# Performance work log

Measured on AMD Instinct MI355X. Metric: run time of the kernel, lower is better.

## Reference

```python
import jax, jax.numpy as jnp
import numpy as np

K = 5  # Chebyshev order


def laplacian(w):
    # normalized Laplacian: I - D^{-1/2} W D^{-1/2}
    d = jnp.sum(w, axis=1)
    d_re = 1.0 / jnp.sqrt(d + 1e-5)
    return jnp.eye(w.shape[0], dtype=w.dtype) - d_re[:, None] * w * d_re[None, :]


def cheb_terms(x, lap, k):
    # x: [B,N,C], lap: [N,N] -> [B,k,N,C]
    # Faithful to torch code: T0 = ones, then (x, lap@x) recurrence for k>2.
    t0 = jnp.ones_like(x)
    if k == 1:
        return t0[:, None]
    t1 = jnp.matmul(lap, x)
    if k == 2:
        return jnp.stack([t0, t1], axis=1)
    terms = [t0, x, t1]
    tkm1, tk = x, t1
    for _ in range(3, k):
        tkm1, tk = tk, 2.0 * jnp.matmul(lap, tk) - tkm1
        terms.append(tk)
    return jnp.stack(terms, axis=1)


def graph_conv(x, lap, w, k):
    # torch: cp.permute(0,2,3,1).flatten(2) @ w, i.e. flat index = c*k + t
    t = cheb_terms(x, lap, k)                       # [B,k,N,C]
    C = x.shape[-1]
    O = w.shape[-1]
    return jnp.einsum('bknc,cko->bno', t, w.reshape(C, k, O))


def setup_inputs() -> dict:
    key = jax.random.key(0)
    ks = jax.random.split(key, 9)
    B, N, Cin, H = 8192, 32, 60, 128
    return {
        'x': jax.random.normal(ks[0], (B, N, Cin), dtype=jnp.float32),
        'adj': jax.random.normal(ks[1], (N, N), dtype=jnp.float32) * 0.1,
        'adj_bias': jax.random.normal(ks[2], (1,), dtype=jnp.float32) * 0.1 + 0.2,
        'w1': jax.random.normal(ks[3], (K * Cin, H), dtype=jnp.float32) * 0.05,
        'b1': jax.random.normal(ks[4], (1, 1, H), dtype=jnp.float32) * 0.05,
        'w2': jax.random.normal(ks[5], (K * H, H), dtype=jnp.float32) * 0.05,
        'b2': jax.random.normal(ks[6], (1, 1, H), dtype=jnp.float32) * 0.05,
        'fc_w': jax.random.normal(ks[7], (2, N * H), dtype=jnp.float32) * 0.02,
        'fc_b': jax.random.normal(ks[8], (2,), dtype=jnp.float32) * 0.02,
    }


def reference(x, adj, adj_bias, w1, b1, w2, b2, fc_w, fc_b):
    # DGCNN.forward (eval mode: dropout = identity)
    a = jax.nn.relu(adj + adj_bias)
    lap = laplacian(a)
    h = graph_conv(x, lap, w1, K)
    h = jax.nn.relu(h + b1)      # B1ReLU
    h = graph_conv(h, lap, w2, K)
    h = jax.nn.relu(h + b2)
    h = h.reshape(h.shape[0], -1)  # [B, N*H]
    return h @ fc_w.T + fc_b
```

## Files before the change

### kernel.cpp

```cpp
#include <hip/hip_runtime.h>

typedef unsigned short u16;
typedef short bf16x8 __attribute__((ext_vector_type(8)));
typedef short short4v __attribute__((ext_vector_type(4)));
typedef float f32x4 __attribute__((ext_vector_type(4)));

#define MFMA16(a, b, c) __builtin_amdgcn_mfma_f32_16x16x32_bf16((a), (b), (c), 0, 0, 0)

__device__ __forceinline__ u16 f2bf(float f) {
  unsigned u = __builtin_bit_cast(unsigned, f);
  u += 0x7FFFu + ((u >> 16) & 1u);
  return (u16)(u >> 16);
}

#define WS_MGF   0
#define WS_WT1F  8192
#define WS_WT2F  73728
#define WS_B1    204800
#define WS_B2    205312

__global__ void prep_kernel(const float* __restrict__ adj,
                            const float* __restrict__ adj_bias,
                            const float* __restrict__ w1,
                            const float* __restrict__ b1,
                            const float* __restrict__ w2,
                            const float* __restrict__ b2,
                            char* __restrict__ ws) {
  const int tid = threadIdx.x;
  if (blockIdx.x == 0) {
    __shared__ float sa[1024], Ls[1024], L2s[1024], L3s[1024], sdre[32];
    float bias = adj_bias[0];
    for (int i = tid; i < 1024; i += 256) sa[i] = fmaxf(adj[i] + bias, 0.0f);
    __syncthreads();
    if (tid < 32) {
      float s = 0.0f;
      for (int c = 0; c < 32; ++c) s += sa[tid * 32 + c];
      sdre[tid] = 1.0f / sqrtf(s + 1e-5f);
    }
    __syncthreads();
    for (int i = tid; i < 1024; i += 256) {
      int n = i >> 5, c = i & 31;
      Ls[i] = (n == c ? 1.0f : 0.0f) - sdre[n] * sa[i] * sdre[c];
    }
    __syncthreads();
    for (int i = tid; i < 1024; i += 256) {
      int r = i >> 5, c = i & 31;
      float s = 0.0f;
      for (int m = 0; m < 32; ++m) s += Ls[r * 32 + m] * Ls[m * 32 + c];
      L2s[i] = s;
    }
    __syncthreads();
    for (int i = tid; i < 1024; i += 256) {
      int r = i >> 5, c = i & 31;
      float s = 0.0f;
      for (int m = 0; m < 32; ++m) s += L2s[r * 32 + m] * Ls[m * 32 + c];
      L3s[i] = s;
    }
    __syncthreads();
    u16* MGf = (u16*)(ws + WS_MGF);
    for (int i = tid; i < 4096; i += 256) {
      int jt = i >> 9, lane = (i >> 3) & 63, j = i & 7;
      int col = jt * 16 + (lane & 15);
      int k = ((lane >> 4) << 3) + j;
      int kk = col >> 5, np = col & 31;
      float v;
      if (kk == 0)      v = (np == k) ? 1.0f : 0.0f;
      else if (kk == 1) v = Ls[np * 32 + k];
      else if (kk == 2) v = 2.0f * L2s[np * 32 + k] - (np == k ? 1.0f : 0.0f);
      else              v = 4.0f * L3s[np * 32 + k] - 3.0f * Ls[np * 32 + k];
      MGf[i] = f2bf(v);
    }
    float* B1 = (float*)(ws + WS_B1);
    float* B2 = (float*)(ws + WS_B2);
    if (tid < 128) {
      float s = b1[tid];
      for (int c = 0; c < 60; ++c) s += w1[(c * 5) * 128 + tid];
      B1[tid] = s;
    } else {
      int o = tid - 128;
      float s = b2[o];
      for (int c = 0; c < 128; ++c) s += w2[(c * 5) * 128 + o];
      B2[o] = s;
    }
  } else {
    u16* WT1F = (u16*)(ws + WS_WT1F);
    u16* WT2F = (u16*)(ws + WS_WT2F);
    int g = (blockIdx.x - 1) * 256 + tid;
    for (int i = g; i < 32768; i += 16 * 256) {
      int ot = i >> 12, ks = (i >> 9) & 7, lane = (i >> 3) & 63, j = i & 7;
      int o = ot * 16 + (lane & 15);
      int kc = ks * 32 + ((lane >> 4) << 3) + j;
      int k = kc >> 6, c = kc & 63;
      WT1F[i] = (c < 60) ? f2bf(w1[(c * 5 + k + 1) * 128 + o]) : (u16)0;
    }
    for (int i = g; i < 65536; i += 16 * 256) {
      int mt = i >> 13, ks = (i >> 9) & 15, lane = (i >> 3) & 63, j = i & 7;
      int o = mt * 16 + (lane & 15);
      int kc = ks * 32 + ((lane >> 4) << 3) + j;
      int k = kc >> 7, c = kc & 127;
      WT2F[i] = f2bf(w2[(c * 5 + k + 1) * 128 + o]);
    }
  }
}

__global__ __launch_bounds__(256, 3) void dgcnn_kernel(
    const float* __restrict__ x,
    const char* __restrict__ ws,
    const float* __restrict__ fc_w,
    const float* __restrict__ fc_b,
    float* __restrict__ out) {
  __shared__ __align__(16) char arena[44032];
  __shared__ float red[8];
  u16* Xt = (u16*)arena;
  u16* Ht = (u16*)arena;
  u16* Y1 = (u16*)(arena + 10752);
  u16* Y2 = (u16*)(arena + 10752);
  float* H2 = (float*)arena;

  const u16* MGf  = (const u16*)(ws + WS_MGF);
  const u16* WT1F = (const u16*)(ws + WS_WT1F);
  const u16* WT2F = (const u16*)(ws + WS_WT2F);
  const float* bias1 = (const float*)(ws + WS_B1);
  const float* bias2 = (const float*)(ws + WS_B2);

  const int tid = threadIdx.x;
  const int w = tid >> 6, lane = tid & 63;
  const int l15 = lane & 15, q = lane >> 4;
  const int b = blockIdx.x;
  const f32x4 z4 = {0.0f, 0.0f, 0.0f, 0.0f};

  for (int i = tid; i < 2560; i += 256) Xt[i] = 0;
  bf16x8 mB0 = *(const bf16x8*)(MGf + ((2 * w + 0) * 64 + lane) * 8);
  bf16x8 mB1 = *(const bf16x8*)(MGf + ((2 * w + 1) * 64 + lane) * 8);
  __syncthreads();
  const float* xb = x + (size_t)b * 1920;
  for (int i = tid; i < 1920; i += 256) {
    int n = i / 60, c = i - n * 60;
    Xt[c * 40 + n] = f2bf(xb[i]);
  }
  __syncthreads();

  {
    f32x4 acc[4][2];
#pragma unroll
    for (int mt = 0; mt < 4; ++mt) {
      bf16x8 aX = *(const bf16x8*)&Xt[(mt * 16 + l15) * 40 + q * 8];
      acc[mt][0] = MFMA16(aX, mB0, z4);
      acc[mt][1] = MFMA16(aX, mB1, z4);
    }
#pragma unroll
    for (int mt = 0; mt < 4; ++mt)
#pragma unroll
      for (int jt = 0; jt < 2; ++jt) {
        int np = jt * 16 + l15;
        int cb = mt * 16 + q * 4;
        short4v v;
        v[0] = (short)f2bf(acc[mt][jt][0]);
        v[1] = (short)f2bf(acc[mt][jt][1]);
        v[2] = (short)f2bf(acc[mt][jt][2]);
        v[3] = (short)f2bf(acc[mt][jt][3]);
        *(short4v*)&Y1[np * 264 + w * 64 + cb] = v;
      }
  }
  __syncthreads();

  {
    f32x4 acc[2][2] = {{z4, z4}, {z4, z4}};
#pragma unroll
    for (int ks = 0; ks < 8; ++ks) {
      bf16x8 a0 = *(const bf16x8*)&Y1[(l15) * 264 + ks * 32 + q * 8];
      bf16x8 a1 = *(const bf16x8*)&Y1[(16 + l15) * 264 + ks * 32 + q * 8];
      bf16x8 b0 = *(const bf16x8*)(WT1F + (((2 * w + 0) * 8 + ks) * 64 + lane) * 8);
      bf16x8 b1 = *(const bf16x8*)(WT1F + (((2 * w + 1) * 8 + ks) * 64 + lane) * 8);
      acc[0][0] = MFMA16(a0, b0, acc[0][0]);
      acc[0][1] = MFMA16(a0, b1, acc[0][1]);
      acc[1][0] = MFMA16(a1, b0, acc[1][0]);
      acc[1][1] = MFMA16(a1, b1, acc[1][1]);
    }
#pragma unroll
    for (int ot = 0; ot < 2; ++ot) {
      int o = (2 * w + ot) * 16 + l15;
      float bv = bias1[o];
#pragma unroll
      for (int mt = 0; mt < 2; ++mt) {
        int nb = mt * 16 + q * 4;
        short4v v;
        v[0] = (short)f2bf(fmaxf(acc[mt][ot][0] + bv, 0.0f));
        v[1] = (short)f2bf(fmaxf(acc[mt][ot][1] + bv, 0.0f));
        v[2] = (short)f2bf(fmaxf(acc[mt][ot][2] + bv, 0.0f));
        v[3] = (short)f2bf(fmaxf(acc[mt][ot][3] + bv, 0.0f));
        *(short4v*)&Ht[o * 40 + nb] = v;
      }
    }
  }
  __syncthreads();

  {
    f32x4 acc[8][2];
#pragma unroll
    for (int mt = 0; mt < 8; ++mt) {
      bf16x8 aH = *(const bf16x8*)&Ht[(mt * 16 + l15) * 40 + q * 8];
      acc[mt][0] = MFMA16(aH, mB0, z4);
      acc[mt][1] = MFMA16(aH, mB1, z4);
    }
#pragma unroll
    for (int mt = 0; mt < 8; ++mt)
#pragma unroll
      for (int jt = 0; jt < 2; ++jt) {
        int np = jt * 16 + l15;
        int ob = mt * 16 + q * 4;
        short4v v;
        v[0] = (short)f2bf(acc[mt][jt][0]);
        v[1] = (short)f2bf(acc[mt][jt][1]);
        v[2] = (short)f2bf(acc[mt][jt][2]);
        v[3] = (short)f2bf(acc[mt][jt][3]);
        *(short4v*)&Y2[np * 520 + w * 128 + ob] = v;
      }
  }
  __syncthreads();

  {
    f32x4 acc[2][2] = {{z4, z4}, {z4, z4}};
#pragma unroll
    for (int ks = 0; ks < 16; ++ks) {
      bf16x8 aw0 = *(const bf16x8*)(WT2F + (((2 * w + 0) * 16 + ks) * 64 + lane) * 8);
      bf16x8 aw1 = *(const bf16x8*)(WT2F + (((2 * w + 1) * 16 + ks) * 64 + lane) * 8);
      bf16x8 by0 = *(const bf16x8*)&Y2[(l15) * 520 + ks * 32 + q * 8];
      bf16x8 by1 = *(const bf16x8*)&Y2[(16 + l15) * 520 + ks * 32 + q * 8];
      acc[0][0] = MFMA16(aw0, by0, acc[0][0]);
      acc[0][1] = MFMA16(aw0, by1, acc[0][1]);
      acc[1][0] = MFMA16(aw1, by0, acc[1][0]);
      acc[1][1] = MFMA16(aw1, by1, acc[1][1]);
    }
    __syncthreads();
#pragma unroll
    for (int ot = 0; ot < 2; ++ot) {
      int ob = (2 * w + ot) * 16 + q * 4;
      float4 bv = *(const float4*)&bias2[ob];
#pragma unroll
      for (int nt = 0; nt < 2; ++nt) {
        int n = nt * 16 + l15;
        float4 hv;
        hv.x = fmaxf(acc[ot][nt][0] + bv.x, 0.0f);
        hv.y = fmaxf(acc[ot][nt][1] + bv.y, 0.0f);
        hv.z = fmaxf(acc[ot][nt][2] + bv.z, 0.0f);
        hv.w = fmaxf(acc[ot][nt][3] + bv.w, 0.0f);
        *(float4*)&H2[n * 132 + ob] = hv;
      }
    }
  }
  __syncthreads();

  float p0 = 0.0f, p1 = 0.0f;
#pragma unroll
  for (int r = 0; r < 16; ++r) {
    int idx = r * 256 + tid;
    float v = H2[(idx >> 7) * 132 + (idx & 127)];
    p0 = fmaf(v, fc_w[idx], p0);
    p1 = fmaf(v, fc_w[4096 + idx], p1);
  }
#pragma unroll
  for (int off = 32; off >= 1; off >>= 1) {
    p0 += __shfl_xor(p0, off);
    p1 += __shfl_xor(p1, off);
  }
  if ((tid & 63) == 0) {
    red[(tid >> 6) * 2 + 0] = p0;
    red[(tid >> 6) * 2 + 1] = p1;
  }
  __syncthreads();
  if (tid < 2) {
    out[b * 2 + tid] = red[tid] + red[2 + tid] + red[4 + tid] + red[6 + tid] + fc_b[tid];
  }
}

extern "C" void kernel_launch(void* const* d_in, const int* in_sizes, int n_in,
                              void* d_out, int out_size, void* d_ws, size_t ws_size,
                              hipStream_t stream) {
  const float* x        = (const float*)d_in[0];
  const float* adj      = (const float*)d_in[1];
  const float* adj_bias = (const float*)d_in[2];
  const float* w1       = (const float*)d_in[3];
  const float* b1       = (const float*)d_in[4];
  const float* w2       = (const float*)d_in[5];
  const float* b2       = (const float*)d_in[6];
  const float* fc_w     = (const float*)d_in[7];
  const float* fc_b     = (const float*)d_in[8];
  float* out = (float*)d_out;
  char* ws   = (char*)d_ws;

  prep_kernel<<<17, 256, 0, stream>>>(adj, adj_bias, w1, b1, w2, b2, ws);
  dgcnn_kernel<<<8192, 256, 0, stream>>>(x, ws, fc_w, fc_b, out);
}
```

Baseline: 215.8 us.

## Split layer-2 Chebyshev GEMM into halves to shrink LDS and raise occupancy

Layer 2 now builds the Chebyshev product and runs the weight GEMM in two halves of the K dimension. A single Y buffer is reused across both halves, and the pre-packed W2 layout is reordered to match. LDS drops from about 44KB to 27KB and launch bounds rise from 3 to 5 blocks per CU. The FC reduction now reads directly from accumulator registers instead of staging H2 through LDS. The change also uses packed bf16 conversion and zeroes only the padding rows of Xt, removing one barrier; the cost is an extra barrier per half and register pressure under the tighter launch bound.

```diff
diff --git a/kernel.cpp b/kernel.cpp
--- a/kernel.cpp
+++ b/kernel.cpp
@@ -1,16 +1,24 @@
 #include <hip/hip_runtime.h>
 
 typedef unsigned short u16;
+typedef unsigned int u32;
 typedef short bf16x8 __attribute__((ext_vector_type(8)));
-typedef short short4v __attribute__((ext_vector_type(4)));
 typedef float f32x4 __attribute__((ext_vector_type(4)));
 
 #define MFMA16(a, b, c) __builtin_amdgcn_mfma_f32_16x16x32_bf16((a), (b), (c), 0, 0, 0)
 
 __device__ __forceinline__ u16 f2bf(float f) {
-  unsigned u = __builtin_bit_cast(unsigned, f);
+  u32 u = __builtin_bit_cast(u32, f);
   u += 0x7FFFu + ((u >> 16) & 1u);
   return (u16)(u >> 16);
+}
+__device__ __forceinline__ u32 pk2bf(float a, float b) {
+#if __has_builtin(__builtin_amdgcn_cvt_pk_bf16_f32)
+  auto v = __builtin_amdgcn_cvt_pk_bf16_f32(a, b);
+  return __builtin_bit_cast(u32, v);
+#else
+  return (u32)f2bf(a) | ((u32)f2bf(b) << 16);
+#endif
 }
 
 #define WS_MGF   0
@@ -94,28 +102,27 @@
       WT1F[i] = (c < 60) ? f2bf(w1[(c * 5 + k + 1) * 128 + o]) : (u16)0;
     }
     for (int i = g; i < 65536; i += 16 * 256) {
-      int mt = i >> 13, ks = (i >> 9) & 15, lane = (i >> 3) & 63, j = i & 7;
-      int o = mt * 16 + (lane & 15);
-      int kc = ks * 32 + ((lane >> 4) << 3) + j;
+      int mt = i >> 13, h = (i >> 12) & 1, ks = (i >> 9) & 7;
+      int lane = (i >> 3) & 63, j = i & 7;
+      int kc = ((ks >> 1) << 7) + ((ks & 1) << 5) + (h << 6) + (((lane >> 4)) << 3) + j;
       int k = kc >> 7, c = kc & 127;
+      int o = (mt << 4) + (lane & 15);
       WT2F[i] = f2bf(w2[(c * 5 + k + 1) * 128 + o]);
     }
   }
 }
 
-__global__ __launch_bounds__(256, 3) void dgcnn_kernel(
+__global__ __launch_bounds__(256, 5) void dgcnn_kernel(
     const float* __restrict__ x,
     const char* __restrict__ ws,
     const float* __restrict__ fc_w,
     const float* __restrict__ fc_b,
     float* __restrict__ out) {
-  __shared__ __align__(16) char arena[44032];
+  __shared__ __align__(16) char arena[27136];
   __shared__ float red[8];
   u16* Xt = (u16*)arena;
   u16* Ht = (u16*)arena;
-  u16* Y1 = (u16*)(arena + 10752);
-  u16* Y2 = (u16*)(arena + 10752);
-  float* H2 = (float*)arena;
+  u16* Y  = (u16*)(arena + 10240);
 
   const u16* MGf  = (const u16*)(ws + WS_MGF);
   const u16* WT1F = (const u16*)(ws + WS_WT1F);
@@ -129,10 +136,9 @@
   const int b = blockIdx.x;
   const f32x4 z4 = {0.0f, 0.0f, 0.0f, 0.0f};
 
-  for (int i = tid; i < 2560; i += 256) Xt[i] = 0;
+  for (int i = tid; i < 160; i += 256) Xt[(60 + (i / 40)) * 40 + (i % 40)] = 0;
   bf16x8 mB0 = *(const bf16x8*)(MGf + ((2 * w + 0) * 64 + lane) * 8);
   bf16x8 mB1 = *(const bf16x8*)(MGf + ((2 * w + 1) * 64 + lane) * 8);
-  __syncthreads();
   const float* xb = x + (size_t)b * 1920;
   for (int i = tid; i < 1920; i += 256) {
     int n = i / 60, c = i - n * 60;
@@ -148,18 +154,16 @@
       acc[mt][0] = MFMA16(aX, mB0, z4);
       acc[mt][1] = MFMA16(aX, mB1, z4);
     }
+    __syncthreads();
 #pragma unroll
     for (int mt = 0; mt < 4; ++mt)
 #pragma unroll
       for (int jt = 0; jt < 2; ++jt) {
         int np = jt * 16 + l15;
-        int cb = mt * 16 + q * 4;
-        short4v v;
-        v[0] = (short)f2bf(acc[mt][jt][0]);
-        v[1] = (short)f2bf(acc[mt][jt][1]);
-        v[2] = (short)f2bf(acc[mt][jt][2]);
-        v[3] = (short)f2bf(acc[mt][jt][3]);
-        *(short4v*)&Y1[np * 264 + w * 64 + cb] = v;
+        uint2 vv;
+        vv.x = pk2bf(acc[mt][jt][0], acc[mt][jt][1]);
+        vv.y = pk2bf(acc[mt][jt][2], acc[mt][jt][3]);
+        *(uint2*)&Y[np * 264 + w * 64 + mt * 16 + q * 4] = vv;
       }
   }
   __syncthreads();
@@ -168,8 +172,8 @@
     f32x4 acc[2][2] = {{z4, z4}, {z4, z4}};
 #pragma unroll
     for (int ks = 0; ks < 8; ++ks) {
-      bf16x8 a0 = *(const bf16x8*)&Y1[(l15) * 264 + ks * 32 + q * 8];
-      bf16x8 a1 = *(const bf16x8*)&Y1[(16 + l15) * 264 + ks * 32 + q * 8];
+      bf16x8 a0 = *(const bf16x8*)&Y[(l15) * 264 + ks * 32 + q * 8];
+      bf16x8 a1 = *(const bf16x8*)&Y[(16 + l15) * 264 + ks * 32 + q * 8];
       bf16x8 b0 = *(const bf16x8*)(WT1F + (((2 * w + 0) * 8 + ks) * 64 + lane) * 8);
       bf16x8 b1 = *(const bf16x8*)(WT1F + (((2 * w + 1) * 8 + ks) * 64 + lane) * 8);
       acc[0][0] = MFMA16(a0, b0, acc[0][0]);
@@ -183,90 +187,79 @@
       float bv = bias1[o];
 #pragma unroll
       for (int mt = 0; mt < 2; ++mt) {
-        int nb = mt * 16 + q * 4;
-        short4v v;
-        v[0] = (short)f2bf(fmaxf(acc[mt][ot][0] + bv, 0.0f));
-        v[1] = (short)f2bf(fmaxf(acc[mt][ot][1] + bv, 0.0f));
-        v[2] = (short)f2bf(fmaxf(acc[mt][ot][2] + bv, 0.0f));
-        v[3] = (short)f2bf(fmaxf(acc[mt][ot][3] + bv, 0.0f));
-        *(short4v*)&Ht[o * 40 + nb] = v;
+        uint2 vv;
+        vv.x = pk2bf(fmaxf(acc[mt][ot][0] + bv, 0.0f), fmaxf(acc[mt][ot][1] + bv, 0.0f));
+        vv.y = pk2bf(fmaxf(acc[mt][ot][2] + bv, 0.0f), fmaxf(acc[mt][ot][3] + bv, 0.0f));
+        *(uint2*)&Ht[o * 40 + mt * 16 + q * 4] = vv;
       }
     }
   }
   __syncthreads();
 
-  {
-    f32x4 acc[8][2];
-#pragma unroll
-    for (int mt = 0; mt < 8; ++mt) {
-      bf16x8 aH = *(const bf16x8*)&Ht[(mt * 16 + l15) * 40 + q * 8];
-      acc[mt][0] = MFMA16(aH, mB0, z4);
-      acc[mt][1] = MFMA16(aH, mB1, z4);
-    }
-#pragma unroll
-    for (int mt = 0; mt < 8; ++mt)
-#pragma unroll
-      for (int jt = 0; jt < 2; ++jt) {
-        int np = jt * 16 + l15;
-        int ob = mt * 16 + q * 4;
-        short4v v;
-        v[0] = (short)f2bf(acc[mt][jt][0]);
-        v[1] = (short)f2bf(acc[mt][jt][1]);
-        v[2] = (short)f2bf(acc[mt][jt][2]);
-        v[3] = (short)f2bf(acc[mt][jt][3]);
-        *(short4v*)&Y2[np * 520 + w * 128 + ob] = v;
+  f32x4 acc2[2][2] = {{z4, z4}, {z4, z4}};
+#pragma unroll
+  for (int h = 0; h < 2; ++h) {
+    {
+      f32x4 acc[4][2];
+#pragma unroll
+      for (int mtl = 0; mtl < 4; ++mtl) {
+        int mt = 4 * h + mtl;
+        bf16x8 aH = *(const bf16x8*)&Ht[(mt * 16 + l15) * 40 + q * 8];
+        acc[mtl][0] = MFMA16(aH, mB0, z4);
+        acc[mtl][1] = MFMA16(aH, mB1, z4);
       }
-  }
-  __syncthreads();
-
-  {
-    f32x4 acc[2][2] = {{z4, z4}, {z4, z4}};
-#pragma unroll
-    for (int ks = 0; ks < 16; ++ks) {
-      bf16x8 aw0 = *(const bf16x8*)(WT2F + (((2 * w + 0) * 16 + ks) * 64 + lane) * 8);
-      bf16x8 aw1 = *(const bf16x8*)(WT2F + (((2 * w + 1) * 16 + ks) * 64 + lane) * 8);
-      bf16x8 by0 = *(const bf16x8*)&Y2[(l15) * 520 + ks * 32 + q * 8];
-      bf16x8 by1 = *(const bf16x8*)&Y2[(16 + l15) * 520 + ks * 32 + q * 8];
-      acc[0][0] = MFMA16(aw0, by0, acc[0][0]);
-      acc[0][1] = MFMA16(aw0, by1, acc[0][1]);
-      acc[1][0] = MFMA16(aw1, by0, acc[1][0]);
-      acc[1][1] = MFMA16(aw1, by1, acc[1][1]);
-    }
-    __syncthreads();
-#pragma unroll
-    for (int ot = 0; ot < 2; ++ot) {
-      int ob = (2 * w + ot) * 16 + q * 4;
-      float4 bv = *(const float4*)&bias2[ob];
-#pragma unroll
-      for (int nt = 0; nt < 2; ++nt) {
-        int n = nt * 16 + l15;
-        float4 hv;
-        hv.x = fmaxf(acc[ot][nt][0] + bv.x, 0.0f);
-        hv.y = fmaxf(acc[ot][nt][1] + bv.y, 0.0f);
-        hv.z = fmaxf(acc[ot][nt][2] + bv.z, 0.0f);
-        hv.w = fmaxf(acc[ot][nt][3] + bv.w, 0.0f);
-        *(float4*)&H2[n * 132 + ob] = hv;
-      }
-    }
-  }
-  __syncthreads();
+#pragma unroll
+      for (int mtl = 0; mtl < 4; ++mtl)
+#pragma unroll
+        for (int jt = 0; jt < 2; ++jt) {
+          int np = jt * 16 + l15;
+          uint2 vv;
+          vv.x = pk2bf(acc[mtl][jt][0], acc[mtl][jt][1]);
+          vv.y = pk2bf(acc[mtl][jt][2], acc[mtl][jt][3]);
+          *(uint2*)&Y[np * 264 + w * 64 + mtl * 16 + q * 4] = vv;
+        }
+    }
+    __syncthreads();
+#pragma unroll
+    for (int ks = 0; ks < 8; ++ks) {
+      bf16x8 aw0 = *(const bf16x8*)(WT2F + ((((2 * w + 0) * 2 + h) * 8 + ks) * 64 + lane) * 8);
+      bf16x8 aw1 = *(const bf16x8*)(WT2F + ((((2 * w + 1) * 2 + h) * 8 + ks) * 64 + lane) * 8);
+      bf16x8 by0 = *(const bf16x8*)&Y[(l15) * 264 + ks * 32 + q * 8];
+      bf16x8 by1 = *(const bf16x8*)&Y[(16 + l15) * 264 + ks * 32 + q * 8];
+      acc2[0][0] = MFMA16(aw0, by0, acc2[0][0]);
+      acc2[0][1] = MFMA16(aw0, by1, acc2[0][1]);
+      acc2[1][0] = MFMA16(aw1, by0, acc2[1][0]);
+      acc2[1][1] = MFMA16(aw1, by1, acc2[1][1]);
+    }
+    __syncthreads();
+  }
 
   float p0 = 0.0f, p1 = 0.0f;
 #pragma unroll
-  for (int r = 0; r < 16; ++r) {
-    int idx = r * 256 + tid;
-    float v = H2[(idx >> 7) * 132 + (idx & 127)];
-    p0 = fmaf(v, fc_w[idx], p0);
-    p1 = fmaf(v, fc_w[4096 + idx], p1);
+  for (int ot = 0; ot < 2; ++ot) {
+    int ob = (2 * w + ot) * 16 + q * 4;
+    float4 bv = *(const float4*)&bias2[ob];
+#pragma unroll
+    for (int nt = 0; nt < 2; ++nt) {
+      int n = nt * 16 + l15;
+      float h0 = fmaxf(acc2[ot][nt][0] + bv.x, 0.0f);
+      float h1 = fmaxf(acc2[ot][nt][1] + bv.y, 0.0f);
+      float h2 = fmaxf(acc2[ot][nt][2] + bv.z, 0.0f);
+      float h3 = fmaxf(acc2[ot][nt][3] + bv.w, 0.0f);
+      float4 w0 = *(const float4*)&fc_w[n * 128 + ob];
+      float4 w1v = *(const float4*)&fc_w[4096 + n * 128 + ob];
+      p0 = fmaf(h0, w0.x, fmaf(h1, w0.y, fmaf(h2, w0.z, fmaf(h3, w0.w, p0))));
+      p1 = fmaf(h0, w1v.x, fmaf(h1, w1v.y, fmaf(h2, w1v.z, fmaf(h3, w1v.w, p1))));
+    }
   }
 #pragma unroll
   for (int off = 32; off >= 1; off >>= 1) {
     p0 += __shfl_xor(p0, off);
     p1 += __shfl_xor(p1, off);
   }
-  if ((tid & 63) == 0) {
-    red[(tid >> 6) * 2 + 0] = p0;
-    red[(tid >> 6) * 2 + 1] = p1;
+  if (lane == 0) {
+    red[w * 2 + 0] = p0;
+    red[w * 2 + 1] = p1;
   }
   __syncthreads();
   if (tid < 2) {
```

New measurement: 206.4 us. -4.4%, faster.
